# Optimization experiments

Measured on AMD Instinct MI355X. Metric: run time of the kernel, lower is better.

The kernel has to match this reference:

```python
import jax, jax.numpy as jnp
import numpy as np

EPS = 1e-8
TOPK = 12  # hard-coded fallback size in SSP_func


def _cosine(a, b):
    # torch F.cosine_similarity(dim=1): dot / (max(||a||,eps) * max(||b||,eps))
    dot = (a * b).sum(axis=1)
    na = jnp.sqrt((a * a).sum(axis=1))
    nb = jnp.sqrt((b * b).sum(axis=1))
    return dot / (jnp.maximum(na, EPS) * jnp.maximum(nb, EPS))


def _proto(feat, pred_c, thres):
    # feat: (B, C, HW); pred_c: (B, HW) probabilities for one class
    B, C, HW = feat.shape
    mask = pred_c > thres                                   # (B, HW)
    cnt = mask.sum(axis=-1)                                 # (B,)
    masked_mean = (feat * mask[:, None, :].astype(feat.dtype)).sum(-1) / \
        jnp.maximum(cnt, 1).astype(feat.dtype)[:, None]      # (B, C)
    # top-k fallback when no element exceeds threshold
    _, idx = jax.lax.top_k(pred_c, TOPK)                    # (B, TOPK)
    idx_b = jnp.broadcast_to(idx[:, None, :], (B, C, TOPK))
    topk_mean = jnp.take_along_axis(feat, idx_b, axis=-1).mean(-1)  # (B, C)
    return jnp.where((cnt > 0)[:, None], masked_mean, topk_mean)


def _minmax(x):
    return (x - x.min()) / (x.max() - x.min())


def enhence_forward(supp_fp, supp_bp, query_fea, tau):
    B, C, H, W = query_fea.shape
    # similarity_func on support prototypes
    sim_fg = _cosine(query_fea, supp_fp)                    # (B, H, W)
    sim_bg = _cosine(query_fea, supp_bp)
    query_out = jnp.stack([sim_bg, sim_fg], axis=1) * 10.0  # (B, 2, H, W)
    # SSP_func: per-sample threshold mask + topk fallback -> prototypes
    pred = jax.nn.softmax(query_out, axis=1).reshape(B, 2, H * W)
    fg_thres = jax.nn.sigmoid(tau)
    feat = query_fea.reshape(B, C, H * W)
    query_fp = _proto(feat, pred[:, 1], fg_thres)[:, :, None, None]       # (B,C,1,1)
    query_bp = _proto(feat, pred[:, 0], 1.0 - fg_thres)[:, :, None, None]
    # activation maps, global min-max normalized, blend
    act = _minmax(_cosine(query_fea, query_fp)[:, None])    # (B,1,H,W)
    deact = _minmax(_cosine(query_fea, query_bp)[:, None])
    out = query_fea * act + query_fea * (1.0 - deact)
    return out, query_fp, query_bp


def setup_inputs() -> dict:
    key = jax.random.key(0)
    k1, k2, k3 = jax.random.split(key, 3)
    B, C, H, W = 16, 512, 64, 64
    return {
        "supp_fp": jax.random.normal(k1, (B, C, 1, 1), dtype=jnp.float32),
        "supp_bp": jax.random.normal(k2, (B, C, 1, 1), dtype=jnp.float32),
        "query_fea": jax.random.normal(k3, (B, C, H, W), dtype=jnp.float32),
        "tau": jnp.float32(0.5),  # nn.Parameter init value in torch
    }


def reference(supp_fp, supp_bp, query_fea, tau):
    return enhence_forward(supp_fp, supp_bp, query_fea, tau)
```

## Files before the change

kernel.cpp:

```cpp
#include <hip/hip_runtime.h>
#include <math.h>

#define BB 16
#define CC 512
#define HWS 4096
#define EPSV 1e-8f
#define TK 12
#define NEGINF (-3.402823466e+38f)
#define CSPLIT 8
#define CCH (CC / CSPLIT)

#define OFF_PFG 0
#define OFF_PBG (BB * HWS)
#define OFF_QN  (2 * BB * HWS)
#define OFF_CF  (3 * BB * HWS)
#define OFF_CB  (4 * BB * HWS)
#define OFF_SN  (5 * BB * HWS)
#define OFF_PN  (OFF_SN + 2 * BB)
#define OFF_CNT (OFF_PN + 2 * BB)
#define OFF_TKI (OFF_CNT + 2 * BB)
#define OFF_BMM (OFF_TKI + 2 * BB * TK)
#define OFF_FMM (OFF_BMM + 64 * 4)
#define OFF_PD1 (OFF_FMM + 4)
#define OFF_PD2 (OFF_PD1 + CSPLIT * BB * HWS)
#define OFF_PQQ (OFF_PD2 + CSPLIT * BB * HWS)

__device__ __forceinline__ float sigmoidf_(float x) { return 1.f / (1.f + expf(-x)); }

__global__ void k0_snorm(const float* __restrict__ sfp, const float* __restrict__ sbp,
                         float* __restrict__ snorm) {
    int b = blockIdx.x;
    int t = threadIdx.x;
    float s1 = 0.f, s2 = 0.f;
    for (int c = t; c < CC; c += 64) {
        float v = sfp[b * CC + c]; s1 += v * v;
        float w = sbp[b * CC + c]; s2 += w * w;
    }
    for (int off = 32; off; off >>= 1) {
        s1 += __shfl_down(s1, off);
        s2 += __shfl_down(s2, off);
    }
    if (t == 0) { snorm[b] = sqrtf(s1); snorm[BB + b] = sqrtf(s2); }
}

__global__ void kz_zero(int* __restrict__ cnts) {
    if (threadIdx.x < 2 * BB) cnts[threadIdx.x] = 0;
}

__global__ void k1_dots(const float* __restrict__ q, const float* __restrict__ sfp,
                        const float* __restrict__ sbp,
                        float* __restrict__ p_df, float* __restrict__ p_db,
                        float* __restrict__ p_qq) {
    int b = blockIdx.z, cs = blockIdx.y;
    int hw4 = blockIdx.x * 256 + threadIdx.x;
    __shared__ float sf[CCH], sb[CCH];
    if (threadIdx.x < CCH) sf[threadIdx.x] = sfp[b * CC + cs * CCH + threadIdx.x];
    else if (threadIdx.x < 2 * CCH) sb[threadIdx.x - CCH] = sbp[b * CC + cs * CCH + (threadIdx.x - CCH)];
    __syncthreads();
    const float4* qp4 = (const float4*)(q + (size_t)b * CC * HWS + (size_t)cs * CCH * HWS) + hw4;
    float4 df = {0, 0, 0, 0}, db = {0, 0, 0, 0}, qq = {0, 0, 0, 0};
#pragma unroll 8
    for (int j = 0; j < CCH; j++) {
        float4 v = qp4[(size_t)j * (HWS / 4)];
        float a = sf[j], c = sb[j];
        df.x += v.x * a; df.y += v.y * a; df.z += v.z * a; df.w += v.w * a;
        db.x += v.x * c; db.y += v.y * c; db.z += v.z * c; db.w += v.w * c;
        qq.x += v.x * v.x; qq.y += v.y * v.y; qq.z += v.z * v.z; qq.w += v.w * v.w;
    }
    size_t o = (size_t)(cs * BB + b) * (HWS / 4) + hw4;
    ((float4*)p_df)[o] = df;
    ((float4*)p_db)[o] = db;
    ((float4*)p_qq)[o] = qq;
}

__global__ void k1b_comb(const float* __restrict__ p_df, const float* __restrict__ p_db,
                         const float* __restrict__ p_qq, const float* __restrict__ snorm,
                         const float* __restrict__ tau,
                         float* __restrict__ pfg, float* __restrict__ pbg,
                         float* __restrict__ qn, int* __restrict__ cnts) {
    int b = blockIdx.y;
    int hw4 = blockIdx.x * 256 + threadIdx.x;
    float4 df = {0, 0, 0, 0}, db = {0, 0, 0, 0}, qq = {0, 0, 0, 0};
    for (int cs = 0; cs < CSPLIT; cs++) {
        size_t o = (size_t)(cs * BB + b) * (HWS / 4) + hw4;
        float4 a = ((const float4*)p_df)[o];
        float4 c = ((const float4*)p_db)[o];
        float4 e = ((const float4*)p_qq)[o];
        df.x += a.x; df.y += a.y; df.z += a.z; df.w += a.w;
        db.x += c.x; db.y += c.y; db.z += c.z; db.w += c.w;
        qq.x += e.x; qq.y += e.y; qq.z += e.z; qq.w += e.w;
    }
    float snf = fmaxf(snorm[b], EPSV), snb = fmaxf(snorm[BB + b], EPSV);
    float thres_fg = sigmoidf_(tau[0]);
    float thres_bg = 1.f - thres_fg;
    float4 opf, opb, oqn;
    int cfg = 0, cbg = 0;
    float dfa[4] = {df.x, df.y, df.z, df.w};
    float dba[4] = {db.x, db.y, db.z, db.w};
    float qqa[4] = {qq.x, qq.y, qq.z, qq.w};
    float pfa[4], pba[4], qna[4];
#pragma unroll
    for (int i = 0; i < 4; i++) {
        float na = sqrtf(qqa[i]);
        float den = fmaxf(na, EPSV);
        float simf = dfa[i] / (den * snf);
        float simb = dba[i] / (den * snb);
        float a = 10.f * simb, c2 = 10.f * simf;
        float m = fmaxf(a, c2);
        float ea = expf(a - m), eb = expf(c2 - m);
        float inv = 1.f / (ea + eb);
        pfa[i] = eb * inv;
        pba[i] = ea * inv;
        qna[i] = na;
        cfg += (pfa[i] > thres_fg) ? 1 : 0;
        cbg += (pba[i] > thres_bg) ? 1 : 0;
    }
    opf = {pfa[0], pfa[1], pfa[2], pfa[3]};
    opb = {pba[0], pba[1], pba[2], pba[3]};
    oqn = {qna[0], qna[1], qna[2], qna[3]};
    size_t o = (size_t)b * (HWS / 4) + hw4;
    ((float4*)pfg)[o] = opf;
    ((float4*)pbg)[o] = opb;
    ((float4*)qn)[o] = oqn;
    for (int off = 32; off; off >>= 1) {
        cfg += __shfl_down(cfg, off);
        cbg += __shfl_down(cbg, off);
    }
    if ((threadIdx.x & 63) == 0) {
        atomicAdd(&cnts[b], cfg);
        atomicAdd(&cnts[BB + b], cbg);
    }
}

__global__ void k2_topk(const float* __restrict__ pfg, const float* __restrict__ pbg,
                        const int* __restrict__ cnts, int* __restrict__ tki) {
    int id = blockIdx.x;
    int cls = id >> 4, b = id & 15;
    if (cnts[cls * BB + b] > 0) return;
    int t = threadIdx.x;
    __shared__ float vals[HWS];
    __shared__ float rv[256];
    __shared__ int   ri[256];
    const float* pr = cls ? pbg : pfg;
    for (int i = t; i < HWS; i += 256) vals[i] = pr[b * HWS + i];
    __syncthreads();
    for (int k = 0; k < TK; k++) {
        float bv = NEGINF; int bi = HWS;
        for (int i = t; i < HWS; i += 256) {
            float v = vals[i];
            if (v > bv) { bv = v; bi = i; }
        }
        rv[t] = bv; ri[t] = bi;
        __syncthreads();
        for (int s = 128; s; s >>= 1) {
            if (t < s) {
                float ov = rv[t + s]; int oi = ri[t + s];
                if (ov > rv[t] || (ov == rv[t] && oi < ri[t])) { rv[t] = ov; ri[t] = oi; }
            }
            __syncthreads();
        }
        if (t == 0) {
            tki[(cls * BB + b) * TK + k] = ri[0];
            vals[ri[0]] = NEGINF;
        }
        __syncthreads();
    }
}

__global__ void k3_proto(const float* __restrict__ q, const float* __restrict__ pfg,
                         const float* __restrict__ pbg, const float* __restrict__ tau,
                         const int* __restrict__ cnts, const int* __restrict__ tki,
                         float* __restrict__ out_fp, float* __restrict__ out_bp) {
    int b = blockIdx.y;
    int wave = threadIdx.x >> 6, lane = threadIdx.x & 63;
    int c = blockIdx.x * 4 + wave;
    float thres_fg = sigmoidf_(tau[0]);
    float thres_bg = 1.f - thres_fg;
    const float* qp = q + (size_t)b * CC * HWS + (size_t)c * HWS;
    const float4* qp4 = (const float4*)qp;
    const float4* pf4 = (const float4*)(pfg + (size_t)b * HWS);
    const float4* pb4 = (const float4*)(pbg + (size_t)b * HWS);
    float sfv = 0.f, sbv = 0.f;
#pragma unroll 4
    for (int j = 0; j < HWS / 256; j++) {
        int i4 = j * 64 + lane;
        float4 v = qp4[i4];
        float4 m1 = pf4[i4];
        float4 m2 = pb4[i4];
        sfv += (m1.x > thres_fg ? v.x : 0.f) + (m1.y > thres_fg ? v.y : 0.f)
             + (m1.z > thres_fg ? v.z : 0.f) + (m1.w > thres_fg ? v.w : 0.f);
        sbv += (m2.x > thres_bg ? v.x : 0.f) + (m2.y > thres_bg ? v.y : 0.f)
             + (m2.z > thres_bg ? v.z : 0.f) + (m2.w > thres_bg ? v.w : 0.f);
    }
    for (int off = 32; off; off >>= 1) {
        sfv += __shfl_down(sfv, off);
        sbv += __shfl_down(sbv, off);
    }
    if (lane == 0) {
        int cntf = cnts[b], cntb = cnts[BB + b];
        float fpv, bpv;
        if (cntf > 0) fpv = sfv / (float)cntf;
        else {
            float tf = 0.f;
            for (int j = 0; j < TK; j++) tf += qp[tki[b * TK + j]];
            fpv = tf / (float)TK;
        }
        if (cntb > 0) bpv = sbv / (float)cntb;
        else {
            float tb = 0.f;
            for (int j = 0; j < TK; j++) tb += qp[tki[(BB + b) * TK + j]];
            bpv = tb / (float)TK;
        }
        out_fp[b * CC + c] = fpv;
        out_bp[b * CC + c] = bpv;
    }
}

__global__ void k3b_pnorm(const float* __restrict__ ofp, const float* __restrict__ obp,
                          float* __restrict__ pnorm) {
    int b = blockIdx.x;
    int t = threadIdx.x;
    float s1 = 0.f, s2 = 0.f;
    for (int c = t; c < CC; c += 64) {
        float v = ofp[b * CC + c]; s1 += v * v;
        float w = obp[b * CC + c]; s2 += w * w;
    }
    for (int off = 32; off; off >>= 1) {
        s1 += __shfl_down(s1, off);
        s2 += __shfl_down(s2, off);
    }
    if (t == 0) { pnorm[b] = sqrtf(s1); pnorm[BB + b] = sqrtf(s2); }
}

__global__ void k4_dots(const float* __restrict__ q, const float* __restrict__ ofp,
                        const float* __restrict__ obp,
                        float* __restrict__ p_df, float* __restrict__ p_db) {
    int b = blockIdx.z, cs = blockIdx.y;
    int hw4 = blockIdx.x * 256 + threadIdx.x;
    __shared__ float pf[CCH], pb[CCH];
    if (threadIdx.x < CCH) pf[threadIdx.x] = ofp[b * CC + cs * CCH + threadIdx.x];
    else if (threadIdx.x < 2 * CCH) pb[threadIdx.x - CCH] = obp[b * CC + cs * CCH + (threadIdx.x - CCH)];
    __syncthreads();
    const float4* qp4 = (const float4*)(q + (size_t)b * CC * HWS + (size_t)cs * CCH * HWS) + hw4;
    float4 df = {0, 0, 0, 0}, db = {0, 0, 0, 0};
#pragma unroll 8
    for (int j = 0; j < CCH; j++) {
        float4 v = qp4[(size_t)j * (HWS / 4)];
        float a = pf[j], c = pb[j];
        df.x += v.x * a; df.y += v.y * a; df.z += v.z * a; df.w += v.w * a;
        db.x += v.x * c; db.y += v.y * c; db.z += v.z * c; db.w += v.w * c;
    }
    size_t o = (size_t)(cs * BB + b) * (HWS / 4) + hw4;
    ((float4*)p_df)[o] = df;
    ((float4*)p_db)[o] = db;
}

__global__ void k4b_comb(const float* __restrict__ p_df, const float* __restrict__ p_db,
                         const float* __restrict__ pnorm, const float* __restrict__ qn,
                         float* __restrict__ cf, float* __restrict__ cb,
                         float* __restrict__ bmm) {
    int b = blockIdx.y;
    int hw4 = blockIdx.x * 256 + threadIdx.x;
    float4 df = {0, 0, 0, 0}, db = {0, 0, 0, 0};
    for (int cs = 0; cs < CSPLIT; cs++) {
        size_t o = (size_t)(cs * BB + b) * (HWS / 4) + hw4;
        float4 a = ((const float4*)p_df)[o];
        float4 c = ((const float4*)p_db)[o];
        df.x += a.x; df.y += a.y; df.z += a.z; df.w += a.w;
        db.x += c.x; db.y += c.y; db.z += c.z; db.w += c.w;
    }
    size_t o = (size_t)b * (HWS / 4) + hw4;
    float4 nv = ((const float4*)qn)[o];
    float pnf = fmaxf(pnorm[b], EPSV), pnb = fmaxf(pnorm[BB + b], EPSV);
    float dfa[4] = {df.x, df.y, df.z, df.w};
    float dba[4] = {db.x, db.y, db.z, db.w};
    float nva[4] = {nv.x, nv.y, nv.z, nv.w};
    float cfa[4], cba[4];
    float mnf = 1e38f, mxf = -1e38f, mnb = 1e38f, mxb = -1e38f;
#pragma unroll
    for (int i = 0; i < 4; i++) {
        float na = fmaxf(nva[i], EPSV);
        cfa[i] = dfa[i] / (na * pnf);
        cba[i] = dba[i] / (na * pnb);
        mnf = fminf(mnf, cfa[i]); mxf = fmaxf(mxf, cfa[i]);
        mnb = fminf(mnb, cba[i]); mxb = fmaxf(mxb, cba[i]);
    }
    float4 ocf = {cfa[0], cfa[1], cfa[2], cfa[3]};
    float4 ocb = {cba[0], cba[1], cba[2], cba[3]};
    ((float4*)cf)[o] = ocf;
    ((float4*)cb)[o] = ocb;
    for (int off = 32; off; off >>= 1) {
        mnf = fminf(mnf, __shfl_down(mnf, off));
        mxf = fmaxf(mxf, __shfl_down(mxf, off));
        mnb = fminf(mnb, __shfl_down(mnb, off));
        mxb = fmaxf(mxb, __shfl_down(mxb, off));
    }
    __shared__ float s4[4][4];
    int wave = threadIdx.x >> 6, lane = threadIdx.x & 63;
    if (lane == 0) { s4[wave][0] = mnf; s4[wave][1] = mxf; s4[wave][2] = mnb; s4[wave][3] = mxb; }
    __syncthreads();
    if (threadIdx.x == 0) {
        float a0 = s4[0][0], a1 = s4[0][1], a2 = s4[0][2], a3 = s4[0][3];
        for (int w = 1; w < 4; w++) {
            a0 = fminf(a0, s4[w][0]);
            a1 = fmaxf(a1, s4[w][1]);
            a2 = fminf(a2, s4[w][2]);
            a3 = fmaxf(a3, s4[w][3]);
        }
        int blk = blockIdx.y * gridDim.x + blockIdx.x;
        bmm[blk * 4 + 0] = a0;
        bmm[blk * 4 + 1] = a1;
        bmm[blk * 4 + 2] = a2;
        bmm[blk * 4 + 3] = a3;
    }
}

__global__ void k5_minmax(const float* __restrict__ bmm, float* __restrict__ fmm) {
    int t = threadIdx.x;
    float mnf = bmm[t * 4 + 0], mxf = bmm[t * 4 + 1];
    float mnb = bmm[t * 4 + 2], mxb = bmm[t * 4 + 3];
    for (int off = 32; off; off >>= 1) {
        mnf = fminf(mnf, __shfl_down(mnf, off));
        mxf = fmaxf(mxf, __shfl_down(mxf, off));
        mnb = fminf(mnb, __shfl_down(mnb, off));
        mxb = fmaxf(mxb, __shfl_down(mxb, off));
    }
    if (t == 0) {
        fmm[0] = mnf;
        fmm[1] = 1.f / (mxf - mnf);
        fmm[2] = mnb;
        fmm[3] = 1.f / (mxb - mnb);
    }
}

__global__ void k6_out(const float* __restrict__ q, const float* __restrict__ cf,
                       const float* __restrict__ cb, const float* __restrict__ fmm,
                       float* __restrict__ out) {
    size_t idx = (size_t)blockIdx.x * 256 + threadIdx.x;
    float minf = fmm[0], rf = fmm[1], minb = fmm[2], rb = fmm[3];
    size_t chan = idx >> 10;
    int h4 = (int)(idx & 1023);
    int b = (int)(chan >> 9);
    float4 qv = ((const float4*)q)[idx];
    float4 c1 = ((const float4*)(cf + (size_t)b * HWS))[h4];
    float4 c2 = ((const float4*)(cb + (size_t)b * HWS))[h4];
    float4 o;
    o.x = qv.x * ((c1.x - minf) * rf) + qv.x * (1.f - (c2.x - minb) * rb);
    o.y = qv.y * ((c1.y - minf) * rf) + qv.y * (1.f - (c2.y - minb) * rb);
    o.z = qv.z * ((c1.z - minf) * rf) + qv.z * (1.f - (c2.z - minb) * rb);
    o.w = qv.w * ((c1.w - minf) * rf) + qv.w * (1.f - (c2.w - minb) * rb);
    ((float4*)out)[idx] = o;
}

extern "C" void kernel_launch(void* const* d_in, const int* in_sizes, int n_in,
                              void* d_out, int out_size, void* d_ws, size_t ws_size,
                              hipStream_t stream) {
    const float* sfp = (const float*)d_in[0];
    const float* sbp = (const float*)d_in[1];
    const float* q   = (const float*)d_in[2];
    const float* tau = (const float*)d_in[3];
    float* out = (float*)d_out;
    float* wsf = (float*)d_ws;

    float* pfg = wsf + OFF_PFG;
    float* pbg = wsf + OFF_PBG;
    float* qn  = wsf + OFF_QN;
    float* cf  = wsf + OFF_CF;
    float* cb  = wsf + OFF_CB;
    float* snorm = wsf + OFF_SN;
    float* pnorm = wsf + OFF_PN;
    int*   cnts  = (int*)(wsf + OFF_CNT);
    int*   tki   = (int*)(wsf + OFF_TKI);
    float* bmm   = wsf + OFF_BMM;
    float* fmm   = wsf + OFF_FMM;
    float* p_df  = wsf + OFF_PD1;
    float* p_db  = wsf + OFF_PD2;
    float* p_qq  = wsf + OFF_PQQ;

    float* out_fp = out + (size_t)BB * CC * HWS;
    float* out_bp = out_fp + BB * CC;

    k0_snorm<<<BB, 64, 0, stream>>>(sfp, sbp, snorm);
    kz_zero<<<1, 64, 0, stream>>>(cnts);
    k1_dots<<<dim3(HWS / 1024, CSPLIT, BB), 256, 0, stream>>>(q, sfp, sbp, p_df, p_db, p_qq);
    k1b_comb<<<dim3(HWS / 1024, BB), 256, 0, stream>>>(p_df, p_db, p_qq, snorm, tau, pfg, pbg, qn, cnts);
    k2_topk<<<32, 256, 0, stream>>>(pfg, pbg, cnts, tki);
    k3_proto<<<dim3(CC / 4, BB), 256, 0, stream>>>(q, pfg, pbg, tau, cnts, tki, out_fp, out_bp);
    k3b_pnorm<<<BB, 64, 0, stream>>>(out_fp, out_bp, pnorm);
    k4_dots<<<dim3(HWS / 1024, CSPLIT, BB), 256, 0, stream>>>(q, out_fp, out_bp, p_df, p_db);
    k4b_comb<<<dim3(HWS / 1024, BB), 256, 0, stream>>>(p_df, p_db, pnorm, qn, cf, cb, bmm);
    k5_minmax<<<1, 64, 0, stream>>>(bmm, fmm);
    k6_out<<<(BB * CC * HWS / 4) / 256, 256, 0, stream>>>(q, cf, cb, fmm, out);
}
```

Baseline: 322.8 us.

## Bitpack threshold masks, fold small reduction kernels into atomics, use nontemporal output

Packs the per-pixel foreground and background threshold results into bitmasks in the combine kernel, so the prototype kernel reads shared-memory bits instead of two float probability maps per channel. It removes the zeroing, prototype-norm and min-max kernels by using atomic float adds for the norms and order-preserving unsigned atomics for the global min and max. It also adds launch bounds and nontemporal loads and stores in the output kernel. The cost is fewer launches and less mask traffic, in exchange for atomic contention and a different summation order for the norms.

```diff
diff --git a/kernel.cpp b/kernel.cpp
--- a/kernel.cpp
+++ b/kernel.cpp
@@ -10,25 +10,43 @@
 #define CSPLIT 8
 #define CCH (CC / CSPLIT)
 
+typedef float f32x4 __attribute__((ext_vector_type(4)));
+
 #define OFF_PFG 0
 #define OFF_PBG (BB * HWS)
 #define OFF_QN  (2 * BB * HWS)
 #define OFF_CF  (3 * BB * HWS)
 #define OFF_CB  (4 * BB * HWS)
 #define OFF_SN  (5 * BB * HWS)
-#define OFF_PN  (OFF_SN + 2 * BB)
-#define OFF_CNT (OFF_PN + 2 * BB)
+#define OFF_PN2 (OFF_SN + 2 * BB)
+#define OFF_CNT (OFF_PN2 + 2 * BB)
 #define OFF_TKI (OFF_CNT + 2 * BB)
-#define OFF_BMM (OFF_TKI + 2 * BB * TK)
-#define OFF_FMM (OFF_BMM + 64 * 4)
-#define OFF_PD1 (OFF_FMM + 4)
+#define OFF_FMMU (OFF_TKI + 2 * BB * TK)
+#define OFF_MFG (OFF_FMMU + 16)
+#define OFF_MBG (OFF_MFG + BB * 128)
+#define OFF_PD1 (OFF_MBG + BB * 128)
 #define OFF_PD2 (OFF_PD1 + CSPLIT * BB * HWS)
 #define OFF_PQQ (OFF_PD2 + CSPLIT * BB * HWS)
 
 __device__ __forceinline__ float sigmoidf_(float x) { return 1.f / (1.f + expf(-x)); }
 
-__global__ void k0_snorm(const float* __restrict__ sfp, const float* __restrict__ sbp,
-                         float* __restrict__ snorm) {
+__device__ __forceinline__ unsigned encf_(float f) {
+    unsigned u = __float_as_uint(f);
+    return (u >> 31) ? ~u : (u | 0x80000000u);
+}
+__device__ __forceinline__ float decf_(unsigned e) {
+    return __uint_as_float((e >> 31) ? (e ^ 0x80000000u) : ~e);
+}
+
+__global__ void k0_init(const float* __restrict__ sfp, const float* __restrict__ sbp,
+                        float* __restrict__ snorm, int* __restrict__ cnts,
+                        float* __restrict__ pn2, unsigned* __restrict__ fmmu) {
+    if (blockIdx.x == BB) {
+        int t = threadIdx.x;
+        if (t < 2 * BB) { cnts[t] = 0; pn2[t] = 0.f; }
+        if (t < 4) fmmu[t] = (t & 1) ? 0u : 0xFFFFFFFFu;
+        return;
+    }
     int b = blockIdx.x;
     int t = threadIdx.x;
     float s1 = 0.f, s2 = 0.f;
@@ -43,11 +61,7 @@
     if (t == 0) { snorm[b] = sqrtf(s1); snorm[BB + b] = sqrtf(s2); }
 }
 
-__global__ void kz_zero(int* __restrict__ cnts) {
-    if (threadIdx.x < 2 * BB) cnts[threadIdx.x] = 0;
-}
-
-__global__ void k1_dots(const float* __restrict__ q, const float* __restrict__ sfp,
+__global__ __launch_bounds__(256) void k1_dots(const float* __restrict__ q, const float* __restrict__ sfp,
                         const float* __restrict__ sbp,
                         float* __restrict__ p_df, float* __restrict__ p_db,
                         float* __restrict__ p_qq) {
@@ -73,13 +87,15 @@
     ((float4*)p_qq)[o] = qq;
 }
 
-__global__ void k1b_comb(const float* __restrict__ p_df, const float* __restrict__ p_db,
+__global__ __launch_bounds__(256) void k1b_comb(const float* __restrict__ p_df, const float* __restrict__ p_db,
                          const float* __restrict__ p_qq, const float* __restrict__ snorm,
                          const float* __restrict__ tau,
                          float* __restrict__ pfg, float* __restrict__ pbg,
-                         float* __restrict__ qn, int* __restrict__ cnts) {
+                         float* __restrict__ qn, int* __restrict__ cnts,
+                         unsigned* __restrict__ mfg, unsigned* __restrict__ mbg) {
     int b = blockIdx.y;
-    int hw4 = blockIdx.x * 256 + threadIdx.x;
+    int tid = threadIdx.x;
+    int hw4 = blockIdx.x * 256 + tid;
     float4 df = {0, 0, 0, 0}, db = {0, 0, 0, 0}, qq = {0, 0, 0, 0};
     for (int cs = 0; cs < CSPLIT; cs++) {
         size_t o = (size_t)(cs * BB + b) * (HWS / 4) + hw4;
@@ -93,12 +109,11 @@
     float snf = fmaxf(snorm[b], EPSV), snb = fmaxf(snorm[BB + b], EPSV);
     float thres_fg = sigmoidf_(tau[0]);
     float thres_bg = 1.f - thres_fg;
-    float4 opf, opb, oqn;
-    int cfg = 0, cbg = 0;
     float dfa[4] = {df.x, df.y, df.z, df.w};
     float dba[4] = {db.x, db.y, db.z, db.w};
     float qqa[4] = {qq.x, qq.y, qq.z, qq.w};
     float pfa[4], pba[4], qna[4];
+    unsigned nf = 0, nb = 0;
 #pragma unroll
     for (int i = 0; i < 4; i++) {
         float na = sqrtf(qqa[i]);
@@ -112,23 +127,38 @@
         pfa[i] = eb * inv;
         pba[i] = ea * inv;
         qna[i] = na;
-        cfg += (pfa[i] > thres_fg) ? 1 : 0;
-        cbg += (pba[i] > thres_bg) ? 1 : 0;
-    }
-    opf = {pfa[0], pfa[1], pfa[2], pfa[3]};
-    opb = {pba[0], pba[1], pba[2], pba[3]};
-    oqn = {qna[0], qna[1], qna[2], qna[3]};
+        nf |= (pfa[i] > thres_fg ? 1u : 0u) << i;
+        nb |= (pba[i] > thres_bg ? 1u : 0u) << i;
+    }
+    float4 opf = {pfa[0], pfa[1], pfa[2], pfa[3]};
+    float4 opb = {pba[0], pba[1], pba[2], pba[3]};
+    float4 oqn = {qna[0], qna[1], qna[2], qna[3]};
     size_t o = (size_t)b * (HWS / 4) + hw4;
     ((float4*)pfg)[o] = opf;
     ((float4*)pbg)[o] = opb;
     ((float4*)qn)[o] = oqn;
+    __shared__ unsigned char nibf[256], nibb[256];
+    nibf[tid] = (unsigned char)nf;
+    nibb[tid] = (unsigned char)nb;
+    int cfg = __popc(nf), cbg = __popc(nb);
     for (int off = 32; off; off >>= 1) {
         cfg += __shfl_down(cfg, off);
         cbg += __shfl_down(cbg, off);
     }
-    if ((threadIdx.x & 63) == 0) {
+    if ((tid & 63) == 0) {
         atomicAdd(&cnts[b], cfg);
         atomicAdd(&cnts[BB + b], cbg);
+    }
+    __syncthreads();
+    if (tid < 32) {
+        unsigned wf = 0, wb = 0;
+#pragma unroll
+        for (int k = 0; k < 8; k++) {
+            wf |= ((unsigned)nibf[tid * 8 + k]) << (4 * k);
+            wb |= ((unsigned)nibb[tid * 8 + k]) << (4 * k);
+        }
+        mfg[b * 128 + blockIdx.x * 32 + tid] = wf;
+        mbg[b * 128 + blockIdx.x * 32 + tid] = wb;
     }
 }
 
@@ -167,30 +197,32 @@
     }
 }
 
-__global__ void k3_proto(const float* __restrict__ q, const float* __restrict__ pfg,
-                         const float* __restrict__ pbg, const float* __restrict__ tau,
+__global__ __launch_bounds__(256) void k3_proto(const float* __restrict__ q,
+                         const unsigned* __restrict__ mfg, const unsigned* __restrict__ mbg,
                          const int* __restrict__ cnts, const int* __restrict__ tki,
-                         float* __restrict__ out_fp, float* __restrict__ out_bp) {
+                         float* __restrict__ out_fp, float* __restrict__ out_bp,
+                         float* __restrict__ pn2) {
     int b = blockIdx.y;
-    int wave = threadIdx.x >> 6, lane = threadIdx.x & 63;
+    int t = threadIdx.x;
+    __shared__ unsigned smf[128], smb[128];
+    if (t < 128) smf[t] = mfg[b * 128 + t];
+    else smb[t - 128] = mbg[b * 128 + (t - 128)];
+    __syncthreads();
+    int wave = t >> 6, lane = t & 63;
     int c = blockIdx.x * 4 + wave;
-    float thres_fg = sigmoidf_(tau[0]);
-    float thres_bg = 1.f - thres_fg;
     const float* qp = q + (size_t)b * CC * HWS + (size_t)c * HWS;
-    const float4* qp4 = (const float4*)qp;
-    const float4* pf4 = (const float4*)(pfg + (size_t)b * HWS);
-    const float4* pb4 = (const float4*)(pbg + (size_t)b * HWS);
+    const f32x4* qp4 = (const f32x4*)qp;
     float sfv = 0.f, sbv = 0.f;
 #pragma unroll 4
     for (int j = 0; j < HWS / 256; j++) {
         int i4 = j * 64 + lane;
-        float4 v = qp4[i4];
-        float4 m1 = pf4[i4];
-        float4 m2 = pb4[i4];
-        sfv += (m1.x > thres_fg ? v.x : 0.f) + (m1.y > thres_fg ? v.y : 0.f)
-             + (m1.z > thres_fg ? v.z : 0.f) + (m1.w > thres_fg ? v.w : 0.f);
-        sbv += (m2.x > thres_bg ? v.x : 0.f) + (m2.y > thres_bg ? v.y : 0.f)
-             + (m2.z > thres_bg ? v.z : 0.f) + (m2.w > thres_bg ? v.w : 0.f);
+        f32x4 v = qp4[i4];
+        unsigned wf = smf[i4 >> 3] >> ((i4 & 7) * 4);
+        unsigned wb = smb[i4 >> 3] >> ((i4 & 7) * 4);
+        sfv += (wf & 1 ? v.x : 0.f) + (wf & 2 ? v.y : 0.f)
+             + (wf & 4 ? v.z : 0.f) + (wf & 8 ? v.w : 0.f);
+        sbv += (wb & 1 ? v.x : 0.f) + (wb & 2 ? v.y : 0.f)
+             + (wb & 4 ? v.z : 0.f) + (wb & 8 ? v.w : 0.f);
     }
     for (int off = 32; off; off >>= 1) {
         sfv += __shfl_down(sfv, off);
@@ -213,26 +245,12 @@
         }
         out_fp[b * CC + c] = fpv;
         out_bp[b * CC + c] = bpv;
-    }
-}
-
-__global__ void k3b_pnorm(const float* __restrict__ ofp, const float* __restrict__ obp,
-                          float* __restrict__ pnorm) {
-    int b = blockIdx.x;
-    int t = threadIdx.x;
-    float s1 = 0.f, s2 = 0.f;
-    for (int c = t; c < CC; c += 64) {
-        float v = ofp[b * CC + c]; s1 += v * v;
-        float w = obp[b * CC + c]; s2 += w * w;
-    }
-    for (int off = 32; off; off >>= 1) {
-        s1 += __shfl_down(s1, off);
-        s2 += __shfl_down(s2, off);
-    }
-    if (t == 0) { pnorm[b] = sqrtf(s1); pnorm[BB + b] = sqrtf(s2); }
-}
-
-__global__ void k4_dots(const float* __restrict__ q, const float* __restrict__ ofp,
+        atomicAdd(&pn2[b], fpv * fpv);
+        atomicAdd(&pn2[BB + b], bpv * bpv);
+    }
+}
+
+__global__ __launch_bounds__(256) void k4_dots(const float* __restrict__ q, const float* __restrict__ ofp,
                         const float* __restrict__ obp,
                         float* __restrict__ p_df, float* __restrict__ p_db) {
     int b = blockIdx.z, cs = blockIdx.y;
@@ -255,10 +273,10 @@
     ((float4*)p_db)[o] = db;
 }
 
-__global__ void k4b_comb(const float* __restrict__ p_df, const float* __restrict__ p_db,
-                         const float* __restrict__ pnorm, const float* __restrict__ qn,
+__global__ __launch_bounds__(256) void k4b_comb(const float* __restrict__ p_df, const float* __restrict__ p_db,
+                         const float* __restrict__ pn2, const float* __restrict__ qn,
                          float* __restrict__ cf, float* __restrict__ cb,
-                         float* __restrict__ bmm) {
+                         unsigned* __restrict__ fmmu) {
     int b = blockIdx.y;
     int hw4 = blockIdx.x * 256 + threadIdx.x;
     float4 df = {0, 0, 0, 0}, db = {0, 0, 0, 0};
@@ -271,7 +289,7 @@
     }
     size_t o = (size_t)b * (HWS / 4) + hw4;
     float4 nv = ((const float4*)qn)[o];
-    float pnf = fmaxf(pnorm[b], EPSV), pnb = fmaxf(pnorm[BB + b], EPSV);
+    float pnf = fmaxf(sqrtf(pn2[b]), EPSV), pnb = fmaxf(sqrtf(pn2[BB + b]), EPSV);
     float dfa[4] = {df.x, df.y, df.z, df.w};
     float dba[4] = {db.x, db.y, db.z, db.w};
     float nva[4] = {nv.x, nv.y, nv.z, nv.w};
@@ -307,49 +325,32 @@
             a2 = fminf(a2, s4[w][2]);
             a3 = fmaxf(a3, s4[w][3]);
         }
-        int blk = blockIdx.y * gridDim.x + blockIdx.x;
-        bmm[blk * 4 + 0] = a0;
-        bmm[blk * 4 + 1] = a1;
-        bmm[blk * 4 + 2] = a2;
-        bmm[blk * 4 + 3] = a3;
-    }
-}
-
-__global__ void k5_minmax(const float* __restrict__ bmm, float* __restrict__ fmm) {
-    int t = threadIdx.x;
-    float mnf = bmm[t * 4 + 0], mxf = bmm[t * 4 + 1];
-    float mnb = bmm[t * 4 + 2], mxb = bmm[t * 4 + 3];
-    for (int off = 32; off; off >>= 1) {
-        mnf = fminf(mnf, __shfl_down(mnf, off));
-        mxf = fmaxf(mxf, __shfl_down(mxf, off));
-        mnb = fminf(mnb, __shfl_down(mnb, off));
-        mxb = fmaxf(mxb, __shfl_down(mxb, off));
-    }
-    if (t == 0) {
-        fmm[0] = mnf;
-        fmm[1] = 1.f / (mxf - mnf);
-        fmm[2] = mnb;
-        fmm[3] = 1.f / (mxb - mnb);
-    }
-}
-
-__global__ void k6_out(const float* __restrict__ q, const float* __restrict__ cf,
-                       const float* __restrict__ cb, const float* __restrict__ fmm,
+        atomicMin(&fmmu[0], encf_(a0));
+        atomicMax(&fmmu[1], encf_(a1));
+        atomicMin(&fmmu[2], encf_(a2));
+        atomicMax(&fmmu[3], encf_(a3));
+    }
+}
+
+__global__ __launch_bounds__(256) void k6_out(const float* __restrict__ q, const float* __restrict__ cf,
+                       const float* __restrict__ cb, const unsigned* __restrict__ fmmu,
                        float* __restrict__ out) {
     size_t idx = (size_t)blockIdx.x * 256 + threadIdx.x;
-    float minf = fmm[0], rf = fmm[1], minb = fmm[2], rb = fmm[3];
+    float mnf = decf_(fmmu[0]), mxf = decf_(fmmu[1]);
+    float mnb = decf_(fmmu[2]), mxb = decf_(fmmu[3]);
+    float rf = 1.f / (mxf - mnf), rb = 1.f / (mxb - mnb);
     size_t chan = idx >> 10;
     int h4 = (int)(idx & 1023);
     int b = (int)(chan >> 9);
-    float4 qv = ((const float4*)q)[idx];
-    float4 c1 = ((const float4*)(cf + (size_t)b * HWS))[h4];
-    float4 c2 = ((const float4*)(cb + (size_t)b * HWS))[h4];
-    float4 o;
-    o.x = qv.x * ((c1.x - minf) * rf) + qv.x * (1.f - (c2.x - minb) * rb);
-    o.y = qv.y * ((c1.y - minf) * rf) + qv.y * (1.f - (c2.y - minb) * rb);
-    o.z = qv.z * ((c1.z - minf) * rf) + qv.z * (1.f - (c2.z - minb) * rb);
-    o.w = qv.w * ((c1.w - minf) * rf) + qv.w * (1.f - (c2.w - minb) * rb);
-    ((float4*)out)[idx] = o;
+    f32x4 qv = __builtin_nontemporal_load((const f32x4*)q + idx);
+    f32x4 c1 = ((const f32x4*)(cf + (size_t)b * HWS))[h4];
+    f32x4 c2 = ((const f32x4*)(cb + (size_t)b * HWS))[h4];
+    f32x4 o;
+    o.x = qv.x * ((c1.x - mnf) * rf) + qv.x * (1.f - (c2.x - mnb) * rb);
+    o.y = qv.y * ((c1.y - mnf) * rf) + qv.y * (1.f - (c2.y - mnb) * rb);
+    o.z = qv.z * ((c1.z - mnf) * rf) + qv.z * (1.f - (c2.z - mnb) * rb);
+    o.w = qv.w * ((c1.w - mnf) * rf) + qv.w * (1.f - (c2.w - mnb) * rb);
+    __builtin_nontemporal_store(o, (f32x4*)out + idx);
 }
 
 extern "C" void kernel_launch(void* const* d_in, const int* in_sizes, int n_in,
@@ -368,11 +369,12 @@
     float* cf  = wsf + OFF_CF;
     float* cb  = wsf + OFF_CB;
     float* snorm = wsf + OFF_SN;
-    float* pnorm = wsf + OFF_PN;
+    float* pn2   = wsf + OFF_PN2;
     int*   cnts  = (int*)(wsf + OFF_CNT);
     int*   tki   = (int*)(wsf + OFF_TKI);
-    float* bmm   = wsf + OFF_BMM;
-    float* fmm   = wsf + OFF_FMM;
+    unsigned* fmmu = (unsigned*)(wsf + OFF_FMMU);
+    unsigned* mfg  = (unsigned*)(wsf + OFF_MFG);
+    unsigned* mbg  = (unsigned*)(wsf + OFF_MBG);
     float* p_df  = wsf + OFF_PD1;
     float* p_db  = wsf + OFF_PD2;
     float* p_qq  = wsf + OFF_PQQ;
@@ -380,15 +382,12 @@
     float* out_fp = out + (size_t)BB * CC * HWS;
     float* out_bp = out_fp + BB * CC;
 
-    k0_snorm<<<BB, 64, 0, stream>>>(sfp, sbp, snorm);
-    kz_zero<<<1, 64, 0, stream>>>(cnts);
+    k0_init<<<BB + 1, 64, 0, stream>>>(sfp, sbp, snorm, cnts, pn2, fmmu);
     k1_dots<<<dim3(HWS / 1024, CSPLIT, BB), 256, 0, stream>>>(q, sfp, sbp, p_df, p_db, p_qq);
-    k1b_comb<<<dim3(HWS / 1024, BB), 256, 0, stream>>>(p_df, p_db, p_qq, snorm, tau, pfg, pbg, qn, cnts);
+    k1b_comb<<<dim3(HWS / 1024, BB), 256, 0, stream>>>(p_df, p_db, p_qq, snorm, tau, pfg, pbg, qn, cnts, mfg, mbg);
     k2_topk<<<32, 256, 0, stream>>>(pfg, pbg, cnts, tki);
-    k3_proto<<<dim3(CC / 4, BB), 256, 0, stream>>>(q, pfg, pbg, tau, cnts, tki, out_fp, out_bp);
-    k3b_pnorm<<<BB, 64, 0, stream>>>(out_fp, out_bp, pnorm);
+    k3_proto<<<dim3(CC / 4, BB), 256, 0, stream>>>(q, mfg, mbg, cnts, tki, out_fp, out_bp, pn2);
     k4_dots<<<dim3(HWS / 1024, CSPLIT, BB), 256, 0, stream>>>(q, out_fp, out_bp, p_df, p_db);
-    k4b_comb<<<dim3(HWS / 1024, BB), 256, 0, stream>>>(p_df, p_db, pnorm, qn, cf, cb, bmm);
-    k5_minmax<<<1, 64, 0, stream>>>(bmm, fmm);
-    k6_out<<<(BB * CC * HWS / 4) / 256, 256, 0, stream>>>(q, cf, cb, fmm, out);
-}
+    k4b_comb<<<dim3(HWS / 1024, BB), 256, 0, stream>>>(p_df, p_db, pn2, qn, cf, cb, fmmu);
+    k6_out<<<(BB * CC * HWS / 4) / 256, 256, 0, stream>>>(q, cf, cb, fmmu, out);
+}
```

New measurement: 411.6 us. 27.5% more time.
